# Kernel tuning notes

Measured on AMD Instinct MI355X. Metric: run time of the kernel, lower is better.

The kernel has to match this reference:

```python
import jax, jax.numpy as jnp
import numpy as np

N_TOKEN = 32000
N_LAYER = 6
N_HEAD = 16
D_MODEL = 1024
D_HEAD = 64
D_INNER = 4096
QLEN = 512
MEM_LEN = 512
BSZ = 8
HD = N_HEAD * D_HEAD
SCALE = 1.0 / float(np.sqrt(D_HEAD))
NEG = -1e30


def _layer_norm(x, g, b, eps=1e-5):
    mu = jnp.mean(x, axis=-1, keepdims=True)
    var = jnp.var(x, axis=-1, keepdims=True)
    return (x - mu) * jax.lax.rsqrt(var + eps) * g + b


def _rel_shift(x):
    # x: [qlen, klen, bsz, n_head] -- TXL relative-position shift
    q, k, b, n = x.shape
    zp = jnp.zeros((q, 1, b, n), x.dtype)
    xp = jnp.concatenate([zp, x], axis=1).reshape(k + 1, q, b, n)
    return xp[1:].reshape(q, k, b, n)


def setup_inputs():
    key = jax.random.key(0)
    ks = jax.random.split(key, 12)
    s = 0.02
    rn = lambda k, *sh: jax.random.normal(k, sh, jnp.float32) * s
    z = lambda *sh: jnp.zeros(sh, jnp.float32)
    o = lambda *sh: jnp.ones(sh, jnp.float32)
    return {
        "data": jax.random.randint(ks[0], (QLEN, BSZ), 0, N_TOKEN),
        "target": jax.random.randint(ks[1], (QLEN, BSZ), 0, N_TOKEN),
        "memory": jax.random.normal(ks[2], (N_LAYER, MEM_LEN, BSZ, D_MODEL), jnp.float32),
        "emb_W": rn(ks[3], N_TOKEN, D_MODEL),  # tied input embedding / softmax head
        "r_w_bias": rn(ks[4], N_HEAD, D_HEAD),
        "r_r_bias": rn(ks[5], N_HEAD, D_HEAD),
        "Wq": rn(ks[6], N_LAYER, D_MODEL, HD),
        "Wkv": rn(ks[7], N_LAYER, D_MODEL, 2 * HD),
        "Wr": rn(ks[8], N_LAYER, D_MODEL, HD),
        "Wo": rn(ks[9], N_LAYER, HD, D_MODEL),
        "W1": rn(ks[10], N_LAYER, D_MODEL, D_INNER),
        "b1": z(N_LAYER, D_INNER),
        "W2": rn(ks[11], N_LAYER, D_INNER, D_MODEL),
        "b2": z(N_LAYER, D_MODEL),
        "ln1_g": o(N_LAYER, D_MODEL),
        "ln1_b": z(N_LAYER, D_MODEL),
        "ln2_g": o(N_LAYER, D_MODEL),
        "ln2_b": z(N_LAYER, D_MODEL),
    }


def _model(data, target, memory, emb_W, r_w_bias, r_r_bias, Wq, Wkv, Wr, Wo,
           W1, b1, W2, b2, ln1_g, ln1_b, ln2_g, ln2_b):
    qlen, bsz = data.shape
    mem = jax.lax.stop_gradient(memory)  # TXL detaches memories
    mlen = mem.shape[1]
    klen = mlen + qlen

    word_emb = emb_W[data]  # [q, b, d]

    # sinusoidal relative positions klen-1 .. 0
    pos_seq = jnp.arange(klen - 1, -1, -1, dtype=word_emb.dtype)
    inv_freq = 1.0 / (10000.0 ** (jnp.arange(0, D_MODEL, 2, dtype=word_emb.dtype) / D_MODEL))
    sin_inp = pos_seq[:, None] * inv_freq[None, :]
    pos = jnp.concatenate([jnp.sin(sin_inp), jnp.cos(sin_inp)], axis=-1)  # [klen, d]

    # causal mask with memory: query i can attend keys j <= i + mlen
    mask = jnp.arange(klen)[None, :] > (jnp.arange(qlen)[:, None] + mlen)  # [q, k]

    core = word_emb
    hids = [core]
    for i in range(N_LAYER):
        x_mem = jnp.concatenate([mem[i], core], axis=0)  # [klen, b, d]
        q = (core @ Wq[i]).reshape(qlen, bsz, N_HEAD, D_HEAD)
        kv = x_mem @ Wkv[i]
        k, v = jnp.split(kv, 2, axis=-1)
        k = k.reshape(klen, bsz, N_HEAD, D_HEAD)
        v = v.reshape(klen, bsz, N_HEAD, D_HEAD)
        r_k = (pos @ Wr[i]).reshape(klen, N_HEAD, D_HEAD)

        AC = jnp.einsum('ibnd,jbnd->ijbn', q + r_w_bias, k)
        BD = _rel_shift(jnp.einsum('ibnd,jnd->ijbn', q + r_r_bias, r_k))
        score = (AC + BD) * SCALE
        score = jnp.where(mask[:, :, None, None], NEG, score)
        prob = jax.nn.softmax(score, axis=1)
        vec = jnp.einsum('ijbn,jbnd->ibnd', prob, v).reshape(qlen, bsz, HD)
        attn_out = vec @ Wo[i]
        core = _layer_norm(core + attn_out, ln1_g[i], ln1_b[i])
        ff = jax.nn.relu(core @ W1[i] + b1[i]) @ W2[i] + b2[i]
        core = _layer_norm(core + ff, ln2_g[i], ln2_b[i])
        hids.append(core)

    # adaptive softmax with cutoffs=[] == full tied softmax
    logits = core @ emb_W.T  # [q, b, V]
    logp = jax.nn.log_softmax(logits, axis=-1)
    loss = -jnp.take_along_axis(logp, target[..., None], axis=-1)[..., 0]  # [q, b]

    new_mems = jnp.stack([
        jnp.concatenate([mem[i], hids[i]], axis=0)[-MEM_LEN:] for i in range(N_LAYER)
    ])
    new_mems = jax.lax.stop_gradient(new_mems)
    return loss, new_mems


def reference(data, target, memory, emb_W, r_w_bias, r_r_bias, Wq, Wkv, Wr, Wo,
              W1, b1, W2, b2, ln1_g, ln1_b, ln2_g, ln2_b):
    return _model(data, target, memory, emb_W, r_w_bias, r_r_bias, Wq, Wkv, Wr, Wo,
                  W1, b1, W2, b2, ln1_g, ln1_b, ln2_g, ln2_b)
```

## Files before the change

### kernel.cpp

```cpp
#include <hip/hip_runtime.h>
#include <hip/hip_bf16.h>
#include <math.h>

#define QLEN   512
#define MLEN   512
#define KLEN   1024
#define BSZ    8
#define NH     16
#define DH     64
#define DM     1024
#define DI     4096
#define NTOK   32000
#define NROW   4096
#define XROW   8192
#define VTILES 500

typedef __hip_bfloat16 bf16;
typedef __attribute__((ext_vector_type(8))) short bf16x8;
typedef __attribute__((ext_vector_type(4))) float f32x4;

__device__ __forceinline__ unsigned short f2b(float x) {
    union { float f; unsigned u; } a; a.f = x;
    unsigned r = a.u + 0x7fffu + ((a.u >> 16) & 1u);
    return (unsigned short)(r >> 16);
}
__device__ __forceinline__ float b2f(unsigned short h) {
    union { unsigned u; float f; } a; a.u = ((unsigned)h) << 16;
    return a.f;
}

__device__ __forceinline__ void gload_lds16(const void* g, void* l) {
    __builtin_amdgcn_global_load_lds(
        (const __attribute__((address_space(1))) unsigned int*)g,
        (__attribute__((address_space(3))) unsigned int*)l, 16, 0, 0);
}

__global__ __launch_bounds__(256) void posb_kernel(unsigned short* __restrict__ posb) {
    int j = blockIdx.x;
    int t = threadIdx.x;
    float p = (float)(1023 - j);
    #pragma unroll
    for (int u = 0; u < 4; u++) {
        int dcol = t + u * 256;
        int k = dcol & 511;
        float invf = expf(-((float)k) * (1.0f / 512.0f) * 9.210340371976184f);
        float a = p * invf;
        posb[j * DM + dcol] = f2b((dcol < 512) ? sinf(a) : cosf(a));
    }
}

__global__ __launch_bounds__(256) void gather_emb(const int* __restrict__ data,
                                                  const float* __restrict__ emb,
                                                  float* __restrict__ out) {
    int row = blockIdx.x;
    int t = threadIdx.x;
    int tok = data[row];
    const float4* src = (const float4*)(emb + (size_t)tok * DM);
    float4* dst = (float4*)(out + (size_t)row * DM);
    dst[t] = src[t];
}

__global__ __launch_bounds__(256) void cast_bf16(const float* __restrict__ src,
                                                 unsigned short* __restrict__ dst, int n4) {
    int i = blockIdx.x * 256 + threadIdx.x;
    if (i < n4) {
        float4 v = ((const float4*)src)[i];
        ushort4 o;
        o.x = f2b(v.x); o.y = f2b(v.y); o.z = f2b(v.z); o.w = f2b(v.w);
        ((ushort4*)dst)[i] = o;
    }
}

__global__ __launch_bounds__(256) void castT_kernel(const float* __restrict__ src,
                                                    unsigned short* __restrict__ dst,
                                                    int K, int N) {
    __shared__ float T[32][33];
    int t = threadIdx.x;
    int k0 = blockIdx.y * 32, n0 = blockIdx.x * 32;
    int r = t >> 3, c4 = (t & 7) * 4;
    float4 v = *(const float4*)(src + (size_t)(k0 + r) * N + n0 + c4);
    T[r][c4 + 0] = v.x; T[r][c4 + 1] = v.y; T[r][c4 + 2] = v.z; T[r][c4 + 3] = v.w;
    __syncthreads();
    ushort4 o;
    o.x = f2b(T[c4 + 0][r]); o.y = f2b(T[c4 + 1][r]);
    o.z = f2b(T[c4 + 2][r]); o.w = f2b(T[c4 + 3][r]);
    *(ushort4*)(dst + (size_t)(n0 + r) * K + k0 + c4) = o;
}

template <bool BIAS, bool RELU, bool OUTBF16, int SPLITK = 1>
__global__ __launch_bounds__(256) void gemm_bt(const unsigned short* __restrict__ A,
                                               const unsigned short* __restrict__ B,
                                               const float* __restrict__ bias,
                                               void* __restrict__ Cout,
                                               int M, int N, int K) {
    __shared__ unsigned short As[128 * 32];
    __shared__ unsigned short Bs[128 * 32];
    int t = threadIdx.x;
    int wave = t >> 6, lane = t & 63;
    int bm = blockIdx.y * 128, bn = blockIdx.x * 128;
    int wm = (wave >> 1) * 64, wn = (wave & 1) * 64;
    int quad = lane >> 4, l16 = lane & 15;

    f32x4 acc[4][4] = {};

    int srow = wave * 32 + (lane >> 2);
    int scol = (lane & 3) * 8;
    const unsigned short* Ag = A + (size_t)(bm + srow) * K + scol;
    const unsigned short* Bg = B + (size_t)(bn + srow) * K + scol;
    unsigned short* Al0 = As + (wave * 32) * 32;
    unsigned short* Al1 = As + (wave * 32 + 16) * 32;
    unsigned short* Bl0 = Bs + (wave * 32) * 32;
    unsigned short* Bl1 = Bs + (wave * 32 + 16) * 32;

    int kchunk = K / SPLITK;
    int k0 = (SPLITK > 1) ? blockIdx.z * kchunk : 0;
    for (int kt = k0; kt < k0 + kchunk; kt += 32) {
        gload_lds16(Ag + kt, Al0);
        gload_lds16(Ag + kt + (size_t)16 * K, Al1);
        gload_lds16(Bg + kt, Bl0);
        gload_lds16(Bg + kt + (size_t)16 * K, Bl1);
        __syncthreads();
        bf16x8 af[4], bfr[4];
        #pragma unroll
        for (int mi = 0; mi < 4; mi++)
            af[mi] = *(const bf16x8*)&As[(wm + mi * 16 + l16) * 32 + quad * 8];
        #pragma unroll
        for (int ni = 0; ni < 4; ni++)
            bfr[ni] = *(const bf16x8*)&Bs[(wn + ni * 16 + l16) * 32 + quad * 8];
        #pragma unroll
        for (int mi = 0; mi < 4; mi++)
            #pragma unroll
            for (int ni = 0; ni < 4; ni++)
                acc[mi][ni] = __builtin_amdgcn_mfma_f32_16x16x32_bf16(
                    af[mi], bfr[ni], acc[mi][ni], 0, 0, 0);
        __syncthreads();
    }

    float* Cf = (float*)Cout + ((SPLITK > 1) ? (size_t)blockIdx.z * M * N : (size_t)0);
    #pragma unroll
    for (int mi = 0; mi < 4; mi++) {
        #pragma unroll
        for (int ni = 0; ni < 4; ni++) {
            int c = bn + wn + ni * 16 + l16;
            float bv = BIAS ? bias[c] : 0.0f;
            #pragma unroll
            for (int reg = 0; reg < 4; reg++) {
                int r = bm + wm + mi * 16 + quad * 4 + reg;
                float x = acc[mi][ni][reg];
                if (BIAS) x += bv;
                if (RELU) x = fmaxf(x, 0.0f);
                if (OUTBF16) ((unsigned short*)Cout)[(size_t)r * N + c] = f2b(x);
                else         Cf[(size_t)r * N + c] = x;
            }
        }
    }
}

__global__ __launch_bounds__(256) void lse_gemm_mfma(const unsigned short* __restrict__ A,
                                                     const unsigned short* __restrict__ B,
                                                     float* __restrict__ pmax,
                                                     float* __restrict__ psum) {
    __shared__ unsigned short As[128 * 32];
    __shared__ unsigned short Bs[128 * 32];
    int t = threadIdx.x;
    int wave = t >> 6, lane = t & 63;
    int bm = blockIdx.x * 128, bn = blockIdx.y * 128;
    int wm = (wave >> 1) * 64;
    int quad = lane >> 4, l16 = lane & 15;
    const int K = 1024;

    f32x4 acc[4][4] = {};

    int srow = wave * 32 + (lane >> 2);
    int scol = (lane & 3) * 8;
    const unsigned short* Ag = A + (size_t)(bm + srow) * K + scol;
    const unsigned short* Bg = B + (size_t)(bn + srow) * K + scol;
    unsigned short* Al0 = As + (wave * 32) * 32;
    unsigned short* Al1 = As + (wave * 32 + 16) * 32;
    unsigned short* Bl0 = Bs + (wave * 32) * 32;
    unsigned short* Bl1 = Bs + (wave * 32 + 16) * 32;
    int wn = (wave & 1) * 64;

    for (int kt = 0; kt < K; kt += 32) {
        gload_lds16(Ag + kt, Al0);
        gload_lds16(Ag + kt + (size_t)16 * K, Al1);
        gload_lds16(Bg + kt, Bl0);
        gload_lds16(Bg + kt + (size_t)16 * K, Bl1);
        __syncthreads();
        bf16x8 af[4], bfr[4];
        #pragma unroll
        for (int mi = 0; mi < 4; mi++)
            af[mi] = *(const bf16x8*)&As[(wm + mi * 16 + l16) * 32 + quad * 8];
        #pragma unroll
        for (int ni = 0; ni < 4; ni++)
            bfr[ni] = *(const bf16x8*)&Bs[(wn + ni * 16 + l16) * 32 + quad * 8];
        #pragma unroll
        for (int mi = 0; mi < 4; mi++)
            #pragma unroll
            for (int ni = 0; ni < 4; ni++)
                acc[mi][ni] = __builtin_amdgcn_mfma_f32_16x16x32_bf16(
                    af[mi], bfr[ni], acc[mi][ni], 0, 0, 0);
        __syncthreads();
    }

    int vt = blockIdx.y * 2 + (wave & 1);
    #pragma unroll
    for (int mi = 0; mi < 4; mi++) {
        #pragma unroll
        for (int reg = 0; reg < 4; reg++) {
            float m = -1e30f;
            #pragma unroll
            for (int ni = 0; ni < 4; ni++) m = fmaxf(m, acc[mi][ni][reg]);
            #pragma unroll
            for (int off = 1; off < 16; off <<= 1) m = fmaxf(m, __shfl_xor(m, off, 64));
            float s = 0.0f;
            #pragma unroll
            for (int ni = 0; ni < 4; ni++) s += __expf(acc[mi][ni][reg] - m);
            #pragma unroll
            for (int off = 1; off < 16; off <<= 1) s += __shfl_xor(s, off, 64);
            if (l16 == 0) {
                int r = bm + wm + mi * 16 + quad * 4 + reg;
                pmax[(size_t)r * VTILES + vt] = m;
                psum[(size_t)r * VTILES + vt] = s;
            }
        }
    }
}

__global__ __launch_bounds__(256) void qprep(const float* __restrict__ kqv,
                                             const float* __restrict__ rwb,
                                             const float* __restrict__ rrb,
                                             unsigned short* __restrict__ qw,
                                             unsigned short* __restrict__ qr) {
    int row = blockIdx.x;
    int t = threadIdx.x;
    int i = row >> 3;
    float4 v = ((const float4*)(kqv + (size_t)(4096 + row) * 3072))[t];
    float4 w = ((const float4*)rwb)[t];
    float4 r = ((const float4*)rrb)[t];
    ushort4 ow, os;
    ow.x = f2b(v.x + w.x); ow.y = f2b(v.y + w.y); ow.z = f2b(v.z + w.z); ow.w = f2b(v.w + w.w);
    os.x = f2b(v.x + r.x); os.y = f2b(v.y + r.y); os.z = f2b(v.z + r.z); os.w = f2b(v.w + r.w);
    ((ushort4*)(qr + (size_t)row * DM))[t] = os;
    int col = t * 4;
    int idx = (col & ~63) + ((col & 63) ^ ((i & 7) << 3));
    *(ushort4*)(qw + (size_t)row * DM + idx) = ow;
}

__global__ __launch_bounds__(256) void kvprep(const float* __restrict__ kqv,
                                              unsigned short* __restrict__ Kh,
                                              unsigned short* __restrict__ Vth) {
    int nb = blockIdx.x, jt = blockIdx.y;
    int n = nb >> 3, b = nb & 7;
    int t = threadIdx.x;
    __shared__ float T[64][65];
    int jj = t >> 2, c4 = (t & 3) * 16;
    int j = jt * 64 + jj;
    const float* src = kqv + (size_t)(j * 8 + b) * 3072 + 1024 + n * 64;
    unsigned short* kdst = Kh + (size_t)nb * 65536 + (size_t)j * 64;
    #pragma unroll
    for (int c = 0; c < 4; c++) {
        float4 k4 = ((const float4*)src)[(c4 >> 2) + c];
        ushort4 o;
        o.x = f2b(k4.x); o.y = f2b(k4.y); o.z = f2b(k4.z); o.w = f2b(k4.w);
        int d = c4 + c * 4;
        *(ushort4*)(kdst + (d ^ ((j & 7) << 3))) = o;
    }
    const float* vsrc = src + 1024;
    #pragma unroll
    for (int c = 0; c < 4; c++) {
        float4 v4 = ((const float4*)vsrc)[(c4 >> 2) + c];
        int d = c4 + c * 4;
        T[jj][d] = v4.x; T[jj][d + 1] = v4.y; T[jj][d + 2] = v4.z; T[jj][d + 3] = v4.w;
    }
    __syncthreads();
    int d = t >> 2, j4 = (t & 3) * 16;
    unsigned short* vrow = Vth + (size_t)nb * 65536 + (size_t)d * 1024 + (size_t)(jt >> 1) * 128;
    #pragma unroll
    for (int c = 0; c < 4; c++) {
        ushort4 o;
        int jb = j4 + c * 4;
        o.x = f2b(T[jb][d]); o.y = f2b(T[jb + 1][d]);
        o.z = f2b(T[jb + 2][d]); o.w = f2b(T[jb + 3][d]);
        int jl = (jt & 1) * 64 + jb;
        *(ushort4*)(vrow + (jl ^ ((d & 7) << 3))) = o;
    }
}

__global__ __launch_bounds__(256) void bd_gemm(const unsigned short* __restrict__ A,
                                               const unsigned short* __restrict__ B,
                                               int ldb,
                                               unsigned short* __restrict__ Bt) {
    __shared__ unsigned short As[128 * 32];
    __shared__ unsigned short Bs[128 * 32];
    int t = threadIdx.x;
    int wave = t >> 6, lane = t & 63;
    int bm = blockIdx.y * 128, bn = blockIdx.x * 128, n = blockIdx.z;
    int wm = (wave >> 1) * 64, wn = (wave & 1) * 64;
    int quad = lane >> 4, l16 = lane & 15;
    f32x4 acc[4][4] = {};
    int srow = wave * 32 + (lane >> 2);
    int scol = (lane & 3) * 8;
    const unsigned short* Ag = A + (size_t)(bm + srow) * DM + n * 64 + scol;
    const unsigned short* Bg = B + (size_t)(bn + srow) * ldb + n * 64 + scol;
    unsigned short* Al0 = As + (wave * 32) * 32;
    unsigned short* Al1 = As + (wave * 32 + 16) * 32;
    unsigned short* Bl0 = Bs + (wave * 32) * 32;
    unsigned short* Bl1 = Bs + (wave * 32 + 16) * 32;

    #pragma unroll
    for (int kt = 0; kt < 64; kt += 32) {
        gload_lds16(Ag + kt, Al0);
        gload_lds16(Ag + kt + (size_t)16 * DM, Al1);
        gload_lds16(Bg + kt, Bl0);
        gload_lds16(Bg + kt + (size_t)16 * ldb, Bl1);
        __syncthreads();
        bf16x8 af[4], bfr[4];
        #pragma unroll
        for (int mi = 0; mi < 4; mi++)
            af[mi] = *(const bf16x8*)&As[(wm + mi * 16 + l16) * 32 + quad * 8];
        #pragma unroll
        for (int ni = 0; ni < 4; ni++)
            bfr[ni] = *(const bf16x8*)&Bs[(wn + ni * 16 + l16) * 32 + quad * 8];
        #pragma unroll
        for (int mi = 0; mi < 4; mi++)
            #pragma unroll
            for (int ni = 0; ni < 4; ni++)
                acc[mi][ni] = __builtin_amdgcn_mfma_f32_16x16x32_bf16(
                    af[mi], bfr[ni], acc[mi][ni], 0, 0, 0);
        __syncthreads();
    }

    #pragma unroll
    for (int mi = 0; mi < 4; mi++) {
        #pragma unroll
        for (int reg = 0; reg < 4; reg++) {
            int r = bm + wm + mi * 16 + quad * 4 + reg;
            int i = r >> 3;
            size_t rowbase = ((size_t)n * 4096 + r) * 1024;
            int sw = (i & 7) << 3;
            #pragma unroll
            for (int ni = 0; ni < 4; ni++) {
                int p = bn + wn + ni * 16 + l16;
                int j = p + i - 511;
                if ((unsigned)j < 1024u)
                    Bt[rowbase + (j & ~127) + ((j & 127) ^ sw)] = f2b(acc[mi][ni][reg]);
            }
        }
    }
}

__global__ __launch_bounds__(256) void flash_attn(const unsigned short* __restrict__ qw_b,
                                                  const unsigned short* __restrict__ Kh,
                                                  const unsigned short* __restrict__ Vth,
                                                  const unsigned short* __restrict__ Bt,
                                                  unsigned short* __restrict__ vecb) {
    int qb = blockIdx.x, b = blockIdx.y, n = blockIdx.z;
    int i0 = qb * 64, nb = n * 8 + b;
    int t = threadIdx.x, wave = t >> 6, lane = t & 63;
    int quad = lane >> 4, l16 = lane & 15;
    int wm = wave * 16;
    __shared__ unsigned short Qw_s[64 * 64];
    __shared__ unsigned short K_s[128 * 64];
    __shared__ unsigned short Vt_s[64 * 128];
    __shared__ unsigned short BD_s[64 * 128];

    {
        const unsigned short* g = qw_b
            + (size_t)((i0 + wave * 16 + (lane >> 3)) * 8 + b) * DM + n * 64 + (lane & 7) * 8;
        unsigned short* l = Qw_s + (wave * 16) * 64;
        gload_lds16(g, l);
        gload_lds16(g + (size_t)64 * DM, l + 8 * 64);
    }

    f32x4 o[4] = {};
    float m_run[4] = { -1e30f, -1e30f, -1e30f, -1e30f };
    float l_run[4] = {};

    int nt = ((i0 + 575) >> 7) + 1;
    for (int jt = 0; jt < nt; jt++) {
        int j0 = jt * 128;
        __syncthreads();
        {
            const unsigned short* g = Kh + (size_t)nb * 65536
                + (size_t)(j0 + wave * 32 + (lane >> 3)) * 64 + (lane & 7) * 8;
            unsigned short* l = K_s + (wave * 32) * 64;
            #pragma unroll
            for (int k = 0; k < 4; k++)
                gload_lds16(g + (size_t)k * 512, l + k * 512);
        }
        {
            const unsigned short* g = Vth + (size_t)nb * 65536
                + (size_t)(wave * 16 + (lane >> 4)) * 1024 + j0 + (lane & 15) * 8;
            unsigned short* l = Vt_s + (wave * 16) * 128;
            #pragma unroll
            for (int k = 0; k < 4; k++)
                gload_lds16(g + (size_t)k * 4096, l + k * 512);
        }
        {
            const unsigned short* g = Bt
                + ((size_t)n * 4096 + (size_t)(i0 + wave * 16 + (lane >> 4)) * 8 + b) * 1024
                + j0 + (lane & 15) * 8;
            unsigned short* l = BD_s + (wave * 16) * 128;
            #pragma unroll
            for (int k = 0; k < 4; k++)
                gload_lds16(g + (size_t)k * 32768, l + k * 512);
        }
        __syncthreads();

        int arow = wm + l16;
        int asw = (arow & 7) << 3;
        bf16x8 aq0 = *(const bf16x8*)&Qw_s[arow * 64 + ((quad * 8) ^ asw)];
        bf16x8 aq1 = *(const bf16x8*)&Qw_s[arow * 64 + ((32 + quad * 8) ^ asw)];
        f32x4 s[8];
        #pragma unroll
        for (int ni = 0; ni < 8; ni++) {
            int krow = ni * 16 + l16;
            int ksw = (krow & 7) << 3;
            bf16x8 b0 = *(const bf16x8*)&K_s[krow * 64 + ((quad * 8) ^ ksw)];
            bf16x8 b1 = *(const bf16x8*)&K_s[krow * 64 + ((32 + quad * 8) ^ ksw)];
            f32x4 z = {};
            z = __builtin_amdgcn_mfma_f32_16x16x32_bf16(aq0, b0, z, 0, 0, 0);
            s[ni] = __builtin_amdgcn_mfma_f32_16x16x32_bf16(aq1, b1, z, 0, 0, 0);
        }

        bool last = (jt == nt - 1);
        #pragma unroll
        for (int reg = 0; reg < 4; reg++) {
            int rl = quad * 4 + reg;
            int rsw = (rl & 7) << 3;
            #pragma unroll
            for (int ni = 0; ni < 8; ni++) {
                int c = ni * 16 + l16;
                float bd = b2f(BD_s[(wm + rl) * 128 + (c ^ rsw)]);
                float v = (s[ni][reg] + bd) * 0.125f;
                if (last && (j0 + c > i0 + wm + rl + 512)) v = -1e30f;
                s[ni][reg] = v;
            }
        }

        #pragma unroll
        for (int reg = 0; reg < 4; reg++) {
            float tm = s[0][reg];
            #pragma unroll
            for (int ni = 1; ni < 8; ni++) tm = fmaxf(tm, s[ni][reg]);
            #pragma unroll
            for (int off = 1; off < 16; off <<= 1) tm = fmaxf(tm, __shfl_xor(tm, off, 64));
            float mn = fmaxf(m_run[reg], tm);
            float alpha = __expf(m_run[reg] - mn);
            m_run[reg] = mn;
            float ts = 0.f;
            #pragma unroll
            for (int ni = 0; ni < 8; ni++) {
                float p = __expf(s[ni][reg] - mn);
                s[ni][reg] = p;
                ts += p;
            }
            #pragma unroll
            for (int off = 1; off < 16; off <<= 1) ts += __shfl_xor(ts, off, 64);
            l_run[reg] = l_run[reg] * alpha + ts;
            #pragma unroll
            for (int di = 0; di < 4; di++) o[di][reg] *= alpha;
        }

        #pragma unroll
        for (int reg = 0; reg < 4; reg++) {
            int rl = quad * 4 + reg;
            int rsw = (rl & 7) << 3;
            #pragma unroll
            for (int ni = 0; ni < 8; ni++) {
                int c = ni * 16 + l16;
                BD_s[(wm + rl) * 128 + (c ^ rsw)] = f2b(s[ni][reg]);
            }
        }

        #pragma unroll
        for (int kk = 0; kk < 4; kk++) {
            int prow = wm + l16;
            bf16x8 ap = *(const bf16x8*)&BD_s[prow * 128 + ((kk * 32 + quad * 8) ^ ((prow & 7) << 3))];
            #pragma unroll
            for (int di = 0; di < 4; di++) {
                int vr = di * 16 + l16;
                bf16x8 bv = *(const bf16x8*)&Vt_s[vr * 128 + ((kk * 32 + quad * 8) ^ ((vr & 7) << 3))];
                o[di] = __builtin_amdgcn_mfma_f32_16x16x32_bf16(ap, bv, o[di], 0, 0, 0);
            }
        }
    }

    #pragma unroll
    for (int reg = 0; reg < 4; reg++) {
        float inv = 1.0f / l_run[reg];
        int r = i0 + wm + quad * 4 + reg;
        #pragma unroll
        for (int di = 0; di < 4; di++) {
            vecb[(size_t)(r * 8 + b) * 1024 + n * 64 + di * 16 + l16] = f2b(o[di][reg] * inv);
        }
    }
}

__global__ __launch_bounds__(256) void add_ln_kernel(const float* __restrict__ x,
                                                     const float* __restrict__ y,
                                                     const float* __restrict__ g,
                                                     const float* __restrict__ bb,
                                                     float* __restrict__ out) {
    int row = blockIdx.x;
    int t = threadIdx.x;
    __shared__ float rs[256], rq[256];
    float v[4];
    float s = 0.f, sq = 0.f;
    #pragma unroll
    for (int u = 0; u < 4; u++) {
        int c = t + u * 256;
        float val = x[(size_t)row * DM + c] + y[(size_t)row * DM + c];
        v[u] = val;
        s += val;
        sq += val * val;
    }
    rs[t] = s;
    rq[t] = sq;
    __syncthreads();
    for (int off = 128; off > 0; off >>= 1) {
        if (t < off) { rs[t] += rs[t + off]; rq[t] += rq[t + off]; }
        __syncthreads();
    }
    float mu = rs[0] * (1.0f / 1024.0f);
    float var = rq[0] * (1.0f / 1024.0f) - mu * mu;
    float rstd = rsqrtf(var + 1e-5f);
    #pragma unroll
    for (int u = 0; u < 4; u++) {
        int c = t + u * 256;
        out[(size_t)row * DM + c] = (v[u] - mu) * rstd * g[c] + bb[c];
    }
}

__global__ __launch_bounds__(256) void add_ln4_kernel(const float* __restrict__ x,
                                                      const float* __restrict__ p,
                                                      const float* __restrict__ bias,
                                                      const float* __restrict__ g,
                                                      const float* __restrict__ bb,
                                                      float* __restrict__ out) {
    const size_t S = (size_t)NROW * DM;
    int row = blockIdx.x;
    int t = threadIdx.x;
    __shared__ float rs[256], rq[256];
    float v[4];
    float s = 0.f, sq = 0.f;
    #pragma unroll
    for (int u = 0; u < 4; u++) {
        int c = t + u * 256;
        size_t idx = (size_t)row * DM + c;
        float val = x[idx] + bias[c] + p[idx] + p[S + idx] + p[2 * S + idx] + p[3 * S + idx];
        v[u] = val;
        s += val;
        sq += val * val;
    }
    rs[t] = s;
    rq[t] = sq;
    __syncthreads();
    for (int off = 128; off > 0; off >>= 1) {
        if (t < off) { rs[t] += rs[t + off]; rq[t] += rq[t + off]; }
        __syncthreads();
    }
    float mu = rs[0] * (1.0f / 1024.0f);
    float var = rq[0] * (1.0f / 1024.0f) - mu * mu;
    float rstd = rsqrtf(var + 1e-5f);
    #pragma unroll
    for (int u = 0; u < 4; u++) {
        int c = t + u * 256;
        out[(size_t)row * DM + c] = (v[u] - mu) * rstd * g[c] + bb[c];
    }
}

__global__ __launch_bounds__(256) void tgt_logit_bf(const unsigned short* __restrict__ core,
                                                    const unsigned short* __restrict__ emb,
                                                    const int* __restrict__ target,
                                                    float* __restrict__ out) {
    int row = blockIdx.x;
    int t = threadIdx.x;
    __shared__ float red[256];
    int tok = target[row];
    const unsigned short* a = core + (size_t)row * DM;
    const unsigned short* e = emb + (size_t)tok * DM;
    float s = 0.f;
    #pragma unroll
    for (int u = 0; u < 4; u++) {
        int c = t + u * 256;
        s += b2f(a[c]) * b2f(e[c]);
    }
    red[t] = s;
    __syncthreads();
    for (int off = 128; off > 0; off >>= 1) {
        if (t < off) red[t] += red[t + off];
        __syncthreads();
    }
    if (t == 0) out[row] = red[0];
}

__global__ __launch_bounds__(256) void lse_reduce_kernel(const float* __restrict__ pmax,
                                                         const float* __restrict__ psum,
                                                         const float* __restrict__ ltgt,
                                                         float* __restrict__ loss) {
    int row = blockIdx.x;
    int t = threadIdx.x;
    __shared__ float red[256];
    float m = -1e30f;
    for (int u = t; u < VTILES; u += 256) m = fmaxf(m, pmax[(size_t)row * VTILES + u]);
    red[t] = m;
    __syncthreads();
    for (int off = 128; off > 0; off >>= 1) {
        if (t < off) red[t] = fmaxf(red[t], red[t + off]);
        __syncthreads();
    }
    float M = red[0];
    __syncthreads();
    float s = 0.f;
    for (int u = t; u < VTILES; u += 256)
        s += psum[(size_t)row * VTILES + u] * __expf(pmax[(size_t)row * VTILES + u] - M);
    red[t] = s;
    __syncthreads();
    for (int off = 128; off > 0; off >>= 1) {
        if (t < off) red[t] += red[t + off];
        __syncthreads();
    }
    if (t == 0) loss[row] = M + logf(red[0]) - ltgt[row];
}

extern "C" void kernel_launch(void* const* d_in, const int* in_sizes, int n_in,
                              void* d_out, int out_size, void* d_ws, size_t ws_size,
                              hipStream_t stream) {
    const int*   data   = (const int*)d_in[0];
    const int*   target = (const int*)d_in[1];
    const float* memory = (const float*)d_in[2];
    const float* embW   = (const float*)d_in[3];
    const float* rwb    = (const float*)d_in[4];
    const float* rrb    = (const float*)d_in[5];
    const float* Wq     = (const float*)d_in[6];
    const float* Wkv    = (const float*)d_in[7];
    const float* Wr     = (const float*)d_in[8];
    const float* Wo     = (const float*)d_in[9];
    const float* W1     = (const float*)d_in[10];
    const float* b1     = (const float*)d_in[11];
    const float* W2     = (const float*)d_in[12];
    const float* b2     = (const float*)d_in[13];
    const float* ln1g   = (const float*)d_in[14];
    const float* ln1b   = (const float*)d_in[15];
    const float* ln2g   = (const float*)d_in[16];
    const float* ln2b   = (const float*)d_in[17];

    float* out  = (float*)d_out;
    float* loss = out;
    float* hids = out + 4096;

    const size_t SZ_CORE = (size_t)NROW * DM;

    const size_t MB = 1024 * 1024;
    char* base = (char*)d_ws;
    unsigned short* posb   = (unsigned short*)(base);
    unsigned short* Vth    = (unsigned short*)(base + 2 * MB);
    unsigned short* Kh     = (unsigned short*)(base + 18 * MB);
    unsigned short* vecb   = (unsigned short*)(base + 34 * MB);
    unsigned short* rkball = (unsigned short*)(base + 42 * MB);
    unsigned short* qw_b   = (unsigned short*)(base + 54 * MB);
    unsigned short* qr_b   = (unsigned short*)(base + 62 * MB);
    float* kqv             = (float*)(base + 70 * MB);
    unsigned short* Bt     = (unsigned short*)(base + 70 * MB);
    unsigned short* wT   = (unsigned short*)(base + 2 * MB);
    unsigned short* actb = (unsigned short*)(base + 10 * MB);
    float* tmp           = (float*)(base + 18 * MB);
    float* cmid          = (float*)(base + 70 * MB);
    unsigned short* h1b  = (unsigned short*)(base + 86 * MB);
    float* w2p           = (float*)(base + 118 * MB);
    float* corefinal     = (float*)(base + 18 * MB);
    unsigned short* wrT  = (unsigned short*)(base + 70 * MB);
    unsigned short* corefnb = actb;
    unsigned short* embWb   = (unsigned short*)(base + 70 * MB);
    float* pmax = (float*)(base + 136 * MB);
    float* psum = (float*)(base + 146 * MB);
    float* ltgt = (float*)(base + 160 * MB);

    posb_kernel<<<KLEN, 256, 0, stream>>>(posb);
    gather_emb<<<NROW, 256, 0, stream>>>(data, embW, hids);

    for (int L = 0; L < 6; L++)
        castT_kernel<<<dim3(32, 32), 256, 0, stream>>>(
            Wr + (size_t)L * DM * DM, wrT + (size_t)L * DM * DM, DM, DM);
    gemm_bt<false, false, true><<<dim3(48, 8), 256, 0, stream>>>(
        posb, wrT, nullptr, rkball, KLEN, 6 * DM, DM);

    for (int L = 0; L < 6; L++) {
        const float* cin = hids + (size_t)L * SZ_CORE;
        float* cout = (L < 5) ? (hids + (size_t)(L + 1) * SZ_CORE) : corefinal;

        unsigned short* xmemb = Kh;
        unsigned short* cinb = xmemb + SZ_CORE;
        cast_bf16<<<4096, 256, 0, stream>>>(memory + (size_t)L * SZ_CORE, xmemb, 1 << 20);
        cast_bf16<<<4096, 256, 0, stream>>>(cin, cinb, 1 << 20);

        castT_kernel<<<dim3(32, 32), 256, 0, stream>>>(Wq + (size_t)L * DM * DM, wT, DM, DM);
        castT_kernel<<<dim3(64, 32), 256, 0, stream>>>(
            Wkv + (size_t)L * DM * 2 * DM, wT + (size_t)DM * DM, DM, 2 * DM);
        gemm_bt<false, false, false><<<dim3(24, 64), 256, 0, stream>>>(
            xmemb, wT, nullptr, kqv, XROW, 3 * DM, DM);

        qprep<<<NROW, 256, 0, stream>>>(kqv, rwb, rrb, qw_b, qr_b);
        kvprep<<<dim3(128, 16), 256, 0, stream>>>(kqv, Kh, Vth);
        bd_gemm<<<dim3(8, 32, 16), 256, 0, stream>>>(qr_b, rkball + (size_t)L * DM, 6 * DM, Bt);
        flash_attn<<<dim3(8, 8, 16), 256, 0, stream>>>(qw_b, Kh, Vth, Bt, vecb);

        castT_kernel<<<dim3(32, 32), 256, 0, stream>>>(Wo + (size_t)L * DM * DM, wT, DM, DM);
        gemm_bt<false, false, false><<<dim3(8, 32), 256, 0, stream>>>(
            vecb, wT, nullptr, tmp, NROW, DM, DM);

        add_ln_kernel<<<NROW, 256, 0, stream>>>(cin, tmp, ln1g + L * DM, ln1b + L * DM, cmid);

        cast_bf16<<<4096, 256, 0, stream>>>(cmid, actb, 1 << 20);
        castT_kernel<<<dim3(128, 32), 256, 0, stream>>>(W1 + (size_t)L * DM * DI, wT, DM, DI);
        gemm_bt<true, true, true><<<dim3(32, 32), 256, 0, stream>>>(
            actb, wT, b1 + (size_t)L * DI, h1b, NROW, DI, DM);

        castT_kernel<<<dim3(32, 128), 256, 0, stream>>>(W2 + (size_t)L * DI * DM, wT, DI, DM);
        gemm_bt<false, false, false, 4><<<dim3(8, 32, 4), 256, 0, stream>>>(
            h1b, wT, nullptr, w2p, NROW, DM, DI);

        add_ln4_kernel<<<NROW, 256, 0, stream>>>(
            cmid, w2p, b2 + (size_t)L * DM, ln2g + L * DM, ln2b + L * DM, cout);
    }

    cast_bf16<<<4096, 256, 0, stream>>>(corefinal, corefnb, 1 << 20);
    cast_bf16<<<32768, 256, 0, stream>>>(embW, embWb, (NTOK * DM) / 4);
    tgt_logit_bf<<<NROW, 256, 0, stream>>>(corefnb, embWb, target, ltgt);
    lse_gemm_mfma<<<dim3(32, 250), 256, 0, stream>>>(corefnb, embWb, pmax, psum);
    lse_reduce_kernel<<<NROW, 256, 0, stream>>>(pmax, psum, ltgt, loss);
}
```

Before: 3.435 ms.

## Fuse QKV epilogue into GEMM, emit bf16 from layernorms, split-K Wo GEMM

Adds a dedicated KQV GEMM that writes the swizzled bf16 Q (with both biases), K and transposed V layouts straight from its epilogue. This removes the fp32 kqv round trip and the separate qprep and kvprep kernels, and skips the Q-class tiles over memory rows. The layernorm kernels and the embedding gather now also write bf16 copies, which drops several cast_bf16 launches. The Wo GEMM uses split-K by 2, with the partial sums added inside the layernorm. The tradeoff is scattered 2-byte stores in the GEMM epilogue and a reshuffled workspace layout.

```diff
diff --git a/kernel.cpp b/kernel.cpp
--- a/kernel.cpp
+++ b/kernel.cpp
@@ -51,13 +51,16 @@
 
 __global__ __launch_bounds__(256) void gather_emb(const int* __restrict__ data,
                                                   const float* __restrict__ emb,
-                                                  float* __restrict__ out) {
+                                                  float* __restrict__ out,
+                                                  unsigned short* __restrict__ outb) {
     int row = blockIdx.x;
     int t = threadIdx.x;
     int tok = data[row];
-    const float4* src = (const float4*)(emb + (size_t)tok * DM);
-    float4* dst = (float4*)(out + (size_t)row * DM);
-    dst[t] = src[t];
+    float4 v = ((const float4*)(emb + (size_t)tok * DM))[t];
+    ((float4*)(out + (size_t)row * DM))[t] = v;
+    ushort4 o;
+    o.x = f2b(v.x); o.y = f2b(v.y); o.z = f2b(v.z); o.w = f2b(v.w);
+    ((ushort4*)(outb + (size_t)row * DM))[t] = o;
 }
 
 __global__ __launch_bounds__(256) void cast_bf16(const float* __restrict__ src,
@@ -156,6 +159,112 @@
     }
 }
 
+__global__ __launch_bounds__(256) void kqv_gemm(const unsigned short* __restrict__ A,
+                                                const unsigned short* __restrict__ B,
+                                                const float* __restrict__ rwb,
+                                                const float* __restrict__ rrb,
+                                                unsigned short* __restrict__ qw,
+                                                unsigned short* __restrict__ qr,
+                                                unsigned short* __restrict__ Kh,
+                                                unsigned short* __restrict__ Vth) {
+    int cls = blockIdx.x >> 3;
+    if (cls == 0 && blockIdx.y < 32) return;
+    __shared__ unsigned short As[128 * 32];
+    __shared__ unsigned short Bs[128 * 32];
+    const int K = 1024;
+    int t = threadIdx.x;
+    int wave = t >> 6, lane = t & 63;
+    int bm = blockIdx.y * 128, bn = blockIdx.x * 128;
+    int wm = (wave >> 1) * 64, wn = (wave & 1) * 64;
+    int quad = lane >> 4, l16 = lane & 15;
+
+    f32x4 acc[4][4] = {};
+
+    int srow = wave * 32 + (lane >> 2);
+    int scol = (lane & 3) * 8;
+    const unsigned short* Ag = A + (size_t)(bm + srow) * K + scol;
+    const unsigned short* Bg = B + (size_t)(bn + srow) * K + scol;
+    unsigned short* Al0 = As + (wave * 32) * 32;
+    unsigned short* Al1 = As + (wave * 32 + 16) * 32;
+    unsigned short* Bl0 = Bs + (wave * 32) * 32;
+    unsigned short* Bl1 = Bs + (wave * 32 + 16) * 32;
+
+    for (int kt = 0; kt < K; kt += 32) {
+        gload_lds16(Ag + kt, Al0);
+        gload_lds16(Ag + kt + (size_t)16 * K, Al1);
+        gload_lds16(Bg + kt, Bl0);
+        gload_lds16(Bg + kt + (size_t)16 * K, Bl1);
+        __syncthreads();
+        bf16x8 af[4], bfr[4];
+        #pragma unroll
+        for (int mi = 0; mi < 4; mi++)
+            af[mi] = *(const bf16x8*)&As[(wm + mi * 16 + l16) * 32 + quad * 8];
+        #pragma unroll
+        for (int ni = 0; ni < 4; ni++)
+            bfr[ni] = *(const bf16x8*)&Bs[(wn + ni * 16 + l16) * 32 + quad * 8];
+        #pragma unroll
+        for (int mi = 0; mi < 4; mi++)
+            #pragma unroll
+            for (int ni = 0; ni < 4; ni++)
+                acc[mi][ni] = __builtin_amdgcn_mfma_f32_16x16x32_bf16(
+                    af[mi], bfr[ni], acc[mi][ni], 0, 0, 0);
+        __syncthreads();
+    }
+
+    if (cls == 0) {
+        #pragma unroll
+        for (int ni = 0; ni < 4; ni++) {
+            int c = bn + wn + ni * 16 + l16;
+            float wv = rwb[c], rv = rrb[c];
+            #pragma unroll
+            for (int mi = 0; mi < 4; mi++) {
+                #pragma unroll
+                for (int reg = 0; reg < 4; reg++) {
+                    int r = bm + wm + mi * 16 + quad * 4 + reg;
+                    int row = r - 4096;
+                    int i = row >> 3;
+                    float x = acc[mi][ni][reg];
+                    qr[(size_t)row * DM + c] = f2b(x + rv);
+                    qw[(size_t)row * DM + (c & ~63) + ((c & 63) ^ ((i & 7) << 3))] = f2b(x + wv);
+                }
+            }
+        }
+    } else if (cls == 1) {
+        #pragma unroll
+        for (int ni = 0; ni < 4; ni++) {
+            int cc = bn + wn + ni * 16 + l16 - 1024;
+            int d = cc & 63, hb = cc >> 6;
+            #pragma unroll
+            for (int mi = 0; mi < 4; mi++) {
+                #pragma unroll
+                for (int reg = 0; reg < 4; reg++) {
+                    int r = bm + wm + mi * 16 + quad * 4 + reg;
+                    int j = r >> 3, nb = hb * 8 + (r & 7);
+                    Kh[(size_t)nb * 65536 + (size_t)j * 64 + (d ^ ((j & 7) << 3))] =
+                        f2b(acc[mi][ni][reg]);
+                }
+            }
+        }
+    } else {
+        #pragma unroll
+        for (int ni = 0; ni < 4; ni++) {
+            int cc = bn + wn + ni * 16 + l16 - 2048;
+            int d = cc & 63, hb = cc >> 6;
+            #pragma unroll
+            for (int mi = 0; mi < 4; mi++) {
+                #pragma unroll
+                for (int reg = 0; reg < 4; reg++) {
+                    int r = bm + wm + mi * 16 + quad * 4 + reg;
+                    int j = r >> 3, nb = hb * 8 + (r & 7);
+                    Vth[(size_t)nb * 65536 + (size_t)d * 1024
+                        + (j & ~127) + ((j & 127) ^ ((d & 7) << 3))] =
+                        f2b(acc[mi][ni][reg]);
+                }
+            }
+        }
+    }
+}
+
 __global__ __launch_bounds__(256) void lse_gemm_mfma(const unsigned short* __restrict__ A,
                                                      const unsigned short* __restrict__ B,
                                                      float* __restrict__ pmax,
@@ -224,66 +333,6 @@
                 psum[(size_t)r * VTILES + vt] = s;
             }
         }
-    }
-}
-
-__global__ __launch_bounds__(256) void qprep(const float* __restrict__ kqv,
-                                             const float* __restrict__ rwb,
-                                             const float* __restrict__ rrb,
-                                             unsigned short* __restrict__ qw,
-                                             unsigned short* __restrict__ qr) {
-    int row = blockIdx.x;
-    int t = threadIdx.x;
-    int i = row >> 3;
-    float4 v = ((const float4*)(kqv + (size_t)(4096 + row) * 3072))[t];
-    float4 w = ((const float4*)rwb)[t];
-    float4 r = ((const float4*)rrb)[t];
-    ushort4 ow, os;
-    ow.x = f2b(v.x + w.x); ow.y = f2b(v.y + w.y); ow.z = f2b(v.z + w.z); ow.w = f2b(v.w + w.w);
-    os.x = f2b(v.x + r.x); os.y = f2b(v.y + r.y); os.z = f2b(v.z + r.z); os.w = f2b(v.w + r.w);
-    ((ushort4*)(qr + (size_t)row * DM))[t] = os;
-    int col = t * 4;
-    int idx = (col & ~63) + ((col & 63) ^ ((i & 7) << 3));
-    *(ushort4*)(qw + (size_t)row * DM + idx) = ow;
-}
-
-__global__ __launch_bounds__(256) void kvprep(const float* __restrict__ kqv,
-                                              unsigned short* __restrict__ Kh,
-                                              unsigned short* __restrict__ Vth) {
-    int nb = blockIdx.x, jt = blockIdx.y;
-    int n = nb >> 3, b = nb & 7;
-    int t = threadIdx.x;
-    __shared__ float T[64][65];
-    int jj = t >> 2, c4 = (t & 3) * 16;
-    int j = jt * 64 + jj;
-    const float* src = kqv + (size_t)(j * 8 + b) * 3072 + 1024 + n * 64;
-    unsigned short* kdst = Kh + (size_t)nb * 65536 + (size_t)j * 64;
-    #pragma unroll
-    for (int c = 0; c < 4; c++) {
-        float4 k4 = ((const float4*)src)[(c4 >> 2) + c];
-        ushort4 o;
-        o.x = f2b(k4.x); o.y = f2b(k4.y); o.z = f2b(k4.z); o.w = f2b(k4.w);
-        int d = c4 + c * 4;
-        *(ushort4*)(kdst + (d ^ ((j & 7) << 3))) = o;
-    }
-    const float* vsrc = src + 1024;
-    #pragma unroll
-    for (int c = 0; c < 4; c++) {
-        float4 v4 = ((const float4*)vsrc)[(c4 >> 2) + c];
-        int d = c4 + c * 4;
-        T[jj][d] = v4.x; T[jj][d + 1] = v4.y; T[jj][d + 2] = v4.z; T[jj][d + 3] = v4.w;
-    }
-    __syncthreads();
-    int d = t >> 2, j4 = (t & 3) * 16;
-    unsigned short* vrow = Vth + (size_t)nb * 65536 + (size_t)d * 1024 + (size_t)(jt >> 1) * 128;
-    #pragma unroll
-    for (int c = 0; c < 4; c++) {
-        ushort4 o;
-        int jb = j4 + c * 4;
-        o.x = f2b(T[jb][d]); o.y = f2b(T[jb + 1][d]);
-        o.z = f2b(T[jb + 2][d]); o.w = f2b(T[jb + 3][d]);
-        int jl = (jt & 1) * 64 + jb;
-        *(ushort4*)(vrow + (jl ^ ((d & 7) << 3))) = o;
     }
 }
 
@@ -498,11 +547,15 @@
     }
 }
 
-__global__ __launch_bounds__(256) void add_ln_kernel(const float* __restrict__ x,
-                                                     const float* __restrict__ y,
-                                                     const float* __restrict__ g,
-                                                     const float* __restrict__ bb,
-                                                     float* __restrict__ out) {
+template <int P, bool BIAS>
+__global__ __launch_bounds__(256) void add_lnp(const float* __restrict__ x,
+                                               const float* __restrict__ p,
+                                               const float* __restrict__ bias,
+                                               const float* __restrict__ g,
+                                               const float* __restrict__ bb,
+                                               float* __restrict__ outf,
+                                               unsigned short* __restrict__ outb) {
+    const size_t S = (size_t)NROW * DM;
     int row = blockIdx.x;
     int t = threadIdx.x;
     __shared__ float rs[256], rq[256];
@@ -511,7 +564,11 @@
     #pragma unroll
     for (int u = 0; u < 4; u++) {
         int c = t + u * 256;
-        float val = x[(size_t)row * DM + c] + y[(size_t)row * DM + c];
+        size_t idx = (size_t)row * DM + c;
+        float val = x[idx];
+        if (BIAS) val += bias[c];
+        #pragma unroll
+        for (int k = 0; k < P; k++) val += p[(size_t)k * S + idx];
         v[u] = val;
         s += val;
         sq += val * val;
@@ -529,45 +586,10 @@
     #pragma unroll
     for (int u = 0; u < 4; u++) {
         int c = t + u * 256;
-        out[(size_t)row * DM + c] = (v[u] - mu) * rstd * g[c] + bb[c];
-    }
-}
-
-__global__ __launch_bounds__(256) void add_ln4_kernel(const float* __restrict__ x,
-                                                      const float* __restrict__ p,
-                                                      const float* __restrict__ bias,
-                                                      const float* __restrict__ g,
-                                                      const float* __restrict__ bb,
-                                                      float* __restrict__ out) {
-    const size_t S = (size_t)NROW * DM;
-    int row = blockIdx.x;
-    int t = threadIdx.x;
-    __shared__ float rs[256], rq[256];
-    float v[4];
-    float s = 0.f, sq = 0.f;
-    #pragma unroll
-    for (int u = 0; u < 4; u++) {
-        int c = t + u * 256;
         size_t idx = (size_t)row * DM + c;
-        float val = x[idx] + bias[c] + p[idx] + p[S + idx] + p[2 * S + idx] + p[3 * S + idx];
-        v[u] = val;
-        s += val;
-        sq += val * val;
-    }
-    rs[t] = s;
-    rq[t] = sq;
-    __syncthreads();
-    for (int off = 128; off > 0; off >>= 1) {
-        if (t < off) { rs[t] += rs[t + off]; rq[t] += rq[t + off]; }
-        __syncthreads();
-    }
-    float mu = rs[0] * (1.0f / 1024.0f);
-    float var = rq[0] * (1.0f / 1024.0f) - mu * mu;
-    float rstd = rsqrtf(var + 1e-5f);
-    #pragma unroll
-    for (int u = 0; u < 4; u++) {
-        int c = t + u * 256;
-        out[(size_t)row * DM + c] = (v[u] - mu) * rstd * g[c] + bb[c];
+        float o = (v[u] - mu) * rstd * g[c] + bb[c];
+        outf[idx] = o;
+        outb[idx] = f2b(o);
     }
 }
 
@@ -656,30 +678,32 @@
     const size_t MB = 1024 * 1024;
     char* base = (char*)d_ws;
     unsigned short* posb   = (unsigned short*)(base);
-    unsigned short* Vth    = (unsigned short*)(base + 2 * MB);
-    unsigned short* Kh     = (unsigned short*)(base + 18 * MB);
-    unsigned short* vecb   = (unsigned short*)(base + 34 * MB);
-    unsigned short* rkball = (unsigned short*)(base + 42 * MB);
-    unsigned short* qw_b   = (unsigned short*)(base + 54 * MB);
-    unsigned short* qr_b   = (unsigned short*)(base + 62 * MB);
-    float* kqv             = (float*)(base + 70 * MB);
+    unsigned short* rkball = (unsigned short*)(base + 2 * MB);
+    unsigned short* qw_b   = (unsigned short*)(base + 14 * MB);
+    unsigned short* qr_b   = (unsigned short*)(base + 22 * MB);
+    unsigned short* wTA    = (unsigned short*)(base + 30 * MB);
+    unsigned short* vecb   = (unsigned short*)(base + 30 * MB);
+    unsigned short* Kh     = (unsigned short*)(base + 38 * MB);
+    unsigned short* Vth    = (unsigned short*)(base + 54 * MB);
     unsigned short* Bt     = (unsigned short*)(base + 70 * MB);
-    unsigned short* wT   = (unsigned short*)(base + 2 * MB);
-    unsigned short* actb = (unsigned short*)(base + 10 * MB);
-    float* tmp           = (float*)(base + 18 * MB);
-    float* cmid          = (float*)(base + 70 * MB);
-    unsigned short* h1b  = (unsigned short*)(base + 86 * MB);
-    float* w2p           = (float*)(base + 118 * MB);
-    float* corefinal     = (float*)(base + 18 * MB);
-    unsigned short* wrT  = (unsigned short*)(base + 70 * MB);
-    unsigned short* corefnb = actb;
-    unsigned short* embWb   = (unsigned short*)(base + 70 * MB);
-    float* pmax = (float*)(base + 136 * MB);
-    float* psum = (float*)(base + 146 * MB);
-    float* ltgt = (float*)(base + 160 * MB);
+    unsigned short* memb   = (unsigned short*)(base + 70 * MB);
+    unsigned short* cinb   = (unsigned short*)(base + 78 * MB);
+    float*          cmid   = (float*)(base + 86 * MB);
+    unsigned short* wrT    = (unsigned short*)(base + 86 * MB);
+    unsigned short* wT     = (unsigned short*)(base + 14 * MB);
+    unsigned short* cmidb  = (unsigned short*)(base + 22 * MB);
+    float*          wop    = (float*)(base + 38 * MB);
+    unsigned short* h1b    = (unsigned short*)(base + 102 * MB);
+    float*          w2p    = (float*)(base + 134 * MB);
+    float*          lnscr  = (float*)(base + 30 * MB);
+    unsigned short* embWb  = (unsigned short*)(base + 86 * MB);
+    float*          pmax   = (float*)(base + 152 * MB);
+    float*          psum   = (float*)(base + 162 * MB);
+    float*          ltgt   = (float*)(base + 172 * MB);
+    unsigned short* corefnb = cinb;
 
     posb_kernel<<<KLEN, 256, 0, stream>>>(posb);
-    gather_emb<<<NROW, 256, 0, stream>>>(data, embW, hids);
+    gather_emb<<<NROW, 256, 0, stream>>>(data, embW, hids, cinb);
 
     for (int L = 0; L < 6; L++)
         castT_kernel<<<dim3(32, 32), 256, 0, stream>>>(
@@ -689,44 +713,38 @@
 
     for (int L = 0; L < 6; L++) {
         const float* cin = hids + (size_t)L * SZ_CORE;
-        float* cout = (L < 5) ? (hids + (size_t)(L + 1) * SZ_CORE) : corefinal;
-
-        unsigned short* xmemb = Kh;
-        unsigned short* cinb = xmemb + SZ_CORE;
-        cast_bf16<<<4096, 256, 0, stream>>>(memory + (size_t)L * SZ_CORE, xmemb, 1 << 20);
-        cast_bf16<<<4096, 256, 0, stream>>>(cin, cinb, 1 << 20);
-
-        castT_kernel<<<dim3(32, 32), 256, 0, stream>>>(Wq + (size_t)L * DM * DM, wT, DM, DM);
+        float* coutf = (L < 5) ? (hids + (size_t)(L + 1) * SZ_CORE) : lnscr;
+
+        cast_bf16<<<4096, 256, 0, stream>>>(memory + (size_t)L * SZ_CORE, memb, 1 << 20);
+
+        castT_kernel<<<dim3(32, 32), 256, 0, stream>>>(Wq + (size_t)L * DM * DM, wTA, DM, DM);
         castT_kernel<<<dim3(64, 32), 256, 0, stream>>>(
-            Wkv + (size_t)L * DM * 2 * DM, wT + (size_t)DM * DM, DM, 2 * DM);
-        gemm_bt<false, false, false><<<dim3(24, 64), 256, 0, stream>>>(
-            xmemb, wT, nullptr, kqv, XROW, 3 * DM, DM);
-
-        qprep<<<NROW, 256, 0, stream>>>(kqv, rwb, rrb, qw_b, qr_b);
-        kvprep<<<dim3(128, 16), 256, 0, stream>>>(kqv, Kh, Vth);
+            Wkv + (size_t)L * DM * 2 * DM, wTA + (size_t)DM * DM, DM, 2 * DM);
+        kqv_gemm<<<dim3(24, 64), 256, 0, stream>>>(
+            memb, wTA, rwb, rrb, qw_b, qr_b, Kh, Vth);
+
         bd_gemm<<<dim3(8, 32, 16), 256, 0, stream>>>(qr_b, rkball + (size_t)L * DM, 6 * DM, Bt);
         flash_attn<<<dim3(8, 8, 16), 256, 0, stream>>>(qw_b, Kh, Vth, Bt, vecb);
 
         castT_kernel<<<dim3(32, 32), 256, 0, stream>>>(Wo + (size_t)L * DM * DM, wT, DM, DM);
-        gemm_bt<false, false, false><<<dim3(8, 32), 256, 0, stream>>>(
-            vecb, wT, nullptr, tmp, NROW, DM, DM);
-
-        add_ln_kernel<<<NROW, 256, 0, stream>>>(cin, tmp, ln1g + L * DM, ln1b + L * DM, cmid);
-
-        cast_bf16<<<4096, 256, 0, stream>>>(cmid, actb, 1 << 20);
+        gemm_bt<false, false, false, 2><<<dim3(8, 32, 2), 256, 0, stream>>>(
+            vecb, wT, nullptr, wop, NROW, DM, DM);
+
+        add_lnp<2, false><<<NROW, 256, 0, stream>>>(
+            cin, wop, nullptr, ln1g + L * DM, ln1b + L * DM, cmid, cmidb);
+
         castT_kernel<<<dim3(128, 32), 256, 0, stream>>>(W1 + (size_t)L * DM * DI, wT, DM, DI);
         gemm_bt<true, true, true><<<dim3(32, 32), 256, 0, stream>>>(
-            actb, wT, b1 + (size_t)L * DI, h1b, NROW, DI, DM);
+            cmidb, wT, b1 + (size_t)L * DI, h1b, NROW, DI, DM);
 
         castT_kernel<<<dim3(32, 128), 256, 0, stream>>>(W2 + (size_t)L * DI * DM, wT, DI, DM);
         gemm_bt<false, false, false, 4><<<dim3(8, 32, 4), 256, 0, stream>>>(
             h1b, wT, nullptr, w2p, NROW, DM, DI);
 
-        add_ln4_kernel<<<NROW, 256, 0, stream>>>(
-            cmid, w2p, b2 + (size_t)L * DM, ln2g + L * DM, ln2b + L * DM, cout);
-    }
-
-    cast_bf16<<<4096, 256, 0, stream>>>(corefinal, corefnb, 1 << 20);
+        add_lnp<4, true><<<NROW, 256, 0, stream>>>(
+            cmid, w2p, b2 + (size_t)L * DM, ln2g + L * DM, ln2b + L * DM, coutf, cinb);
+    }
+
     cast_bf16<<<32768, 256, 0, stream>>>(embW, embWb, (NTOK * DM) / 4);
     tgt_logit_bf<<<NROW, 256, 0, stream>>>(corefnb, embWb, target, ltgt);
     lse_gemm_mfma<<<dim3(32, 250), 256, 0, stream>>>(corefnb, embWb, pmax, psum);
```

After: 3.494 ms. About the same (+1.7%).
